# Performance work log

Hardware: AMD Instinct MI355X
Metric: run time of the kernel (lower is better)

The kernel has to match this reference:

```python
import jax, jax.numpy as jnp
import numpy as np

INFLUENCE_RADIUS = 8  # VectorizedTrajectoryComputer default


def compute_trajectories(emb):
    # emb: [B, S, D] -> [B, S, D]
    B, S, D = emb.shape
    diffs = emb[:, 1:] - emb[:, :-1]                      # [B, S-1, D]
    mag = jnp.linalg.norm(diffs, axis=-1, keepdims=True)  # [B, S-1, 1]
    ntraj = diffs / jnp.maximum(mag, 1e-8)                # normalized trajectories
    mw = jnp.tanh(mag[..., 0])                            # magnitude weights [B, S-1]
    pos = jnp.arange(S)[:, None]                          # [S, 1]
    j = jnp.arange(S - 1)[None, :]                        # [1, S-1]
    ws = jnp.maximum(0, pos - INFLUENCE_RADIUS)           # window start per pos
    mask = (j >= ws) & (j < pos)                          # window_end = pos (pos <= S-1)
    wsz = jnp.maximum(pos - ws, 1)                        # window size (>=1 to avoid /0)
    recency = jnp.where(mask, (j - ws + 1) / wsz, 0.0).astype(emb.dtype)  # [S, S-1]
    cw = mw[:, None, :] * recency[None]                   # combined weights [B, S, S-1]
    nw = cw / jnp.maximum(cw.sum(-1, keepdims=True), 1e-8)
    return jnp.einsum('bpj,bjd->bpd', nw, ntraj)          # [B, S, D]


def setup_inputs() -> dict:
    key = jax.random.key(0)
    ks = jax.random.split(key, 6)
    B, S, D = 2, 2048, 1024
    H, K, hd = 16, 16, 64
    return {
        'x': jax.random.normal(ks[0], (B, S, D), dtype=jnp.float32),
        'qkv_w': jax.random.normal(ks[1], (3 * D, D), dtype=jnp.float32) * 0.02,
        'out_w': jax.random.normal(ks[2], (D, D), dtype=jnp.float32) * 0.02,
        'splat_centers': jax.random.normal(ks[3], (H, K, hd), dtype=jnp.float32) * 0.02,
        'splat_log_scales': jnp.zeros((H, K), dtype=jnp.float32),
        'splat_amplitudes': jnp.ones((H, K), dtype=jnp.float32),
    }


def reference(x, qkv_w, out_w, splat_centers, splat_log_scales, splat_amplitudes):
    B, S, D = x.shape
    H, K, hd = splat_centers.shape
    # trajectories (computed when trajectories=None in forward)
    traj = compute_trajectories(x)
    # qkv projection (no bias)
    qkv = x @ qkv_w.T                                      # [B, S, 3D]
    q, k, v = jnp.split(qkv, 3, axis=-1)
    def heads(t):
        return t.reshape(B, S, H, hd).transpose(0, 2, 1, 3)  # [B, H, S, hd]
    q, k, v = heads(q), heads(k), heads(v)
    # squared distances to splat centers: [B, H, S, K]
    cn = jnp.sum(splat_centers ** 2, axis=-1)              # [H, K]
    def dists_sq(t):
        tn = jnp.sum(t ** 2, axis=-1, keepdims=True)       # [B, H, S, 1]
        cross = jnp.einsum('bhsd,hkd->bhsk', t, splat_centers)
        return tn - 2.0 * cross + cn[None, :, None, :]
    scales_sq = jnp.exp(splat_log_scales)[None, :, None, :] ** 2  # [1, H, 1, K]
    amp = jax.nn.sigmoid(splat_amplitudes)[None, :, None, :]
    q_weights = jnp.exp(-0.5 * dists_sq(q) / scales_sq) * amp     # [B, H, S, K]
    k_weights = jnp.exp(-0.5 * dists_sq(k) / scales_sq) * amp
    attn = jnp.einsum('bhis,bhjs->bhij', q_weights, k_weights)    # [B, H, S, S]
    attn = jax.nn.softmax(attn, axis=-1)
    out = jnp.einsum('bhij,bhjd->bhid', attn, v)                  # [B, H, S, hd]
    out = out.transpose(0, 2, 1, 3).reshape(B, S, D) @ out_w.T    # [B, S, D]
    return out, traj
```

## Files before the change

kernel.cpp:

```cpp
#include <hip/hip_runtime.h>
#include <math.h>

#define SEQ 2048
#define DIM 1024
#define NB  2
#define NH  16

typedef __attribute__((ext_vector_type(8))) short short8;
typedef __attribute__((ext_vector_type(4))) float floatx4;
typedef __attribute__((ext_vector_type(16))) float floatx16;

__device__ __forceinline__ ushort f2bf(float f) {
    unsigned u = __float_as_uint(f);
    return (ushort)((u + 0x7FFFu + ((u >> 16) & 1u)) >> 16);
}
__device__ __forceinline__ float bf2f(ushort h) {
    return __uint_as_float(((unsigned)h) << 16);
}
__device__ __forceinline__ void gload16(const void* g, char* lds_base) {
    __builtin_amdgcn_global_load_lds(
        (const __attribute__((address_space(1))) void*)g,
        (__attribute__((address_space(3))) void*)lds_base, 16, 0, 0);
}
__device__ __forceinline__ unsigned cvtpk(float a, float b) {
    unsigned r;
    asm("v_cvt_pk_bf16_f32 %0, %1, %2" : "=v"(r) : "v"(a), "v"(b));
    return r;
}
__device__ __forceinline__ void plswap(unsigned &a, unsigned &b) {
    asm("v_permlane32_swap_b32 %0, %1" : "+v"(a), "+v"(b));
}

__global__ __launch_bounds__(256) void front_kernel(
    const float* __restrict__ x, const float* __restrict__ qkv_w,
    const float* __restrict__ out_w,
    ushort* __restrict__ xh, ushort* __restrict__ xl,
    ushort* __restrict__ wh, ushort* __restrict__ wlv,
    ushort* __restrict__ owh, ushort* __restrict__ owl,
    float* __restrict__ sbuf, float* __restrict__ invbuf)
{
    const int blk = blockIdx.x;
    if (blk < 4096) {
        int i = blk * 1024 + threadIdx.x * 4;
        float4 v = *(const float4*)(x + i);
        ushort4 h, l;
        h.x = f2bf(v.x); l.x = f2bf(v.x - bf2f(h.x));
        h.y = f2bf(v.y); l.y = f2bf(v.y - bf2f(h.y));
        h.z = f2bf(v.z); l.z = f2bf(v.z - bf2f(h.z));
        h.w = f2bf(v.w); l.w = f2bf(v.w - bf2f(h.w));
        *(ushort4*)(xh + i) = h;
        *(ushort4*)(xl + i) = l;
    } else if (blk < 6144) {
        int i = (blk - 4096) * 1024 + threadIdx.x * 4;
        float4 v = *(const float4*)(qkv_w + i);
        ushort4 o;
        o.x = f2bf(v.x); o.y = f2bf(v.y); o.z = f2bf(v.z); o.w = f2bf(v.w);
        *(ushort4*)(wh + i) = o;
    } else if (blk < 7168) {
        int i = (blk - 6144) * 1024 + threadIdx.x * 4;
        float4 v = *(const float4*)(qkv_w + 2097152 + i);
        ushort4 h, l;
        h.x = f2bf(v.x); l.x = f2bf(v.x - bf2f(h.x));
        h.y = f2bf(v.y); l.y = f2bf(v.y - bf2f(h.y));
        h.z = f2bf(v.z); l.z = f2bf(v.z - bf2f(h.z));
        h.w = f2bf(v.w); l.w = f2bf(v.w - bf2f(h.w));
        *(ushort4*)(wh + 2097152 + i) = h;
        *(ushort4*)(wlv + i) = l;
    } else if (blk < 8192) {
        const int wave = threadIdx.x >> 6;
        const int lane = threadIdx.x & 63;
        const int row  = (blk - 7168) * 4 + wave;
        const int NR = NB * (SEQ - 1);
        if (row >= NR) return;
        const int b = row / (SEQ - 1);
        const int j = row - b * (SEQ - 1);
        const float* x0 = x + ((size_t)(b * SEQ + j)) * DIM;
        const float* x1 = x0 + DIM;
        float sum = 0.f;
        #pragma unroll
        for (int q = 0; q < 4; ++q) {
            int idx = q * 256 + lane * 4;
            float4 a = *(const float4*)(x0 + idx);
            float4 c = *(const float4*)(x1 + idx);
            float dx = c.x-a.x, dy = c.y-a.y, dz = c.z-a.z, dw = c.w-a.w;
            sum += dx*dx + dy*dy + dz*dz + dw*dw;
        }
        #pragma unroll
        for (int off = 32; off > 0; off >>= 1) sum += __shfl_down(sum, off);
        if (lane == 0) {
            float mag = sqrtf(sum);
            sbuf[row]   = tanhf(mag);
            invbuf[row] = 1.0f / fmaxf(mag, 1e-8f);
        }
    } else {
        int i = (blk - 8192) * 1024 + threadIdx.x * 4;
        float4 v = *(const float4*)(out_w + i);
        ushort4 h, l;
        h.x = f2bf(v.x); l.x = f2bf(v.x - bf2f(h.x));
        h.y = f2bf(v.y); l.y = f2bf(v.y - bf2f(h.y));
        h.z = f2bf(v.z); l.z = f2bf(v.z - bf2f(h.z));
        h.w = f2bf(v.w); l.w = f2bf(v.w - bf2f(h.w));
        *(ushort4*)(owh + i) = h;
        *(ushort4*)(owl + i) = l;
    }
}

__device__ __forceinline__ void traj_body(
    int bp, const float* __restrict__ x, const float* __restrict__ sbuf,
    const float* __restrict__ invbuf, float* __restrict__ traj_out)
{
    const int b  = bp >> 11;
    const int p  = bp & (SEQ - 1);
    int ws = p - 8; if (ws < 0) ws = 0;
    const int wlen = p - ws;
    const float wsz = (float)((p - ws) > 1 ? (p - ws) : 1);
    const int base = b * (SEQ - 1) + ws;

    float Z = 0.f;
    for (int t = 0; t < wlen; ++t)
        Z += sbuf[base + t] * ((float)(t + 1) / wsz);
    const float scale = 1.0f / fmaxf(Z, 1e-8f);

    const int d0 = threadIdx.x * 4;
    const float* xb = x + ((size_t)(b * SEQ + ws)) * DIM + d0;
    float4 prev = *(const float4*)xb;
    float4 acc = make_float4(0.f,0.f,0.f,0.f);
    for (int t = 0; t < wlen; ++t) {
        xb += DIM;
        float4 cur = *(const float4*)xb;
        float cc = sbuf[base + t] * ((float)(t + 1) / wsz) * invbuf[base + t] * scale;
        acc.x += cc * (cur.x - prev.x);
        acc.y += cc * (cur.y - prev.y);
        acc.z += cc * (cur.z - prev.z);
        acc.w += cc * (cur.w - prev.w);
        prev = cur;
    }
    *(float4*)(traj_out + (size_t)bp * DIM + d0) = acc;
}

template<int SPLIT, int EPI, int BN>
__device__ __forceinline__ void gemm_body(
    int bx, int by, char* smem,
    const ushort* __restrict__ Ah, const ushort* __restrict__ Al,
    const ushort* __restrict__ Bh, const ushort* __restrict__ Bl,
    float* __restrict__ cout, int ldc,
    ushort* __restrict__ qwb)
{
    constexpr int JT   = BN / 32;
    constexpr int BSZ  = BN * 64;
    constexpr int HALF = 8192 + BSZ;
    const int tid = threadIdx.x;
    const int l = tid & 63;
    const int w = tid >> 6;
    const int wm = w >> 1, wn = w & 1;
    const int n0 = bx * BN;
    const int m0 = by * 128;

    char* a_h = smem;
    char* b_h = smem + 8192;
    char* a_l = smem + HALF;
    char* b_l = smem + HALF + 8192;

    const int srowA = 32 * w + (l >> 2);
    const int srowB = (BN == 128 ? 32 * w : 16 * w) + (l >> 2);
    const int scol  = (l & 3) * 8;
    const ushort* Ahg = Ah + (size_t)(m0 + srowA) * 1024 + scol;
    const ushort* Bhg = Bh + (size_t)(n0 + srowB) * 1024 + scol;
    const ushort* Alg = SPLIT ? Al + (size_t)(m0 + srowA) * 1024 + scol : nullptr;
    const ushort* Blg = SPLIT ? Bl + (size_t)(n0 + srowB) * 1024 + scol : nullptr;

    floatx4 acc[4][JT] = {};
    const int fr = l & 15;
    const int fq = (l >> 4) * 16;

    for (int kb = 0; kb < 1024; kb += 32) {
        if (kb) __syncthreads();
        gload16(Ahg + kb,             a_h + w*2048);
        gload16(Ahg + kb + 16*1024,   a_h + w*2048 + 1024);
        if (BN == 128) {
            gload16(Bhg + kb,             b_h + w*2048);
            gload16(Bhg + kb + 16*1024,   b_h + w*2048 + 1024);
        } else {
            gload16(Bhg + kb,             b_h + w*1024);
        }
        if (SPLIT) {
            gload16(Alg + kb,           a_l + w*2048);
            gload16(Alg + kb + 16*1024, a_l + w*2048 + 1024);
            if (BN == 128) {
                gload16(Blg + kb,           b_l + w*2048);
                gload16(Blg + kb + 16*1024, b_l + w*2048 + 1024);
            } else {
                gload16(Blg + kb,           b_l + w*1024);
            }
        }
        __syncthreads();
        short8 fah[4], fbh[JT], fal[4], fbl[JT];
        #pragma unroll
        for (int t = 0; t < 4; ++t) {
            fah[t] = *(const short8*)(a_h + ((wm*64 + t*16 + fr) << 6) + fq);
            if (SPLIT)
                fal[t] = *(const short8*)(a_l + ((wm*64 + t*16 + fr) << 6) + fq);
        }
        #pragma unroll
        for (int t = 0; t < JT; ++t) {
            fbh[t] = *(const short8*)(b_h + ((wn*(BN/2) + t*16 + fr) << 6) + fq);
            if (SPLIT)
                fbl[t] = *(const short8*)(b_l + ((wn*(BN/2) + t*16 + fr) << 6) + fq);
        }
        #pragma unroll
        for (int it = 0; it < 4; ++it)
            #pragma unroll
            for (int jt = 0; jt < JT; ++jt) {
                acc[it][jt] = __builtin_amdgcn_mfma_f32_16x16x32_bf16(
                    fah[it], fbh[jt], acc[it][jt], 0, 0, 0);
                if (SPLIT) {
                    acc[it][jt] = __builtin_amdgcn_mfma_f32_16x16x32_bf16(
                        fah[it], fbl[jt], acc[it][jt], 0, 0, 0);
                    acc[it][jt] = __builtin_amdgcn_mfma_f32_16x16x32_bf16(
                        fal[it], fbh[jt], acc[it][jt], 0, 0, 0);
                }
            }
    }

    const int row0 = (l >> 4) * 4;
    const int col  = l & 15;

    if (EPI == 0) {
        #pragma unroll
        for (int it = 0; it < 4; ++it)
            #pragma unroll
            for (int jt = 0; jt < JT; ++jt)
                #pragma unroll
                for (int r = 0; r < 4; ++r) {
                    int gm = m0 + wm*64 + it*16 + row0 + r;
                    int gn = n0 + wn*(BN/2) + jt*16 + col;
                    cout[(size_t)gm * ldc + gn] = acc[it][jt][r];
                }
    } else {
        #pragma unroll
        for (int it = 0; it < 4; ++it)
            #pragma unroll
            for (int jt = 0; jt < JT; ++jt)
                #pragma unroll
                for (int r = 0; r < 4; ++r) {
                    int md = m0 + wm*64 + it*16 + row0 + r;
                    int t  = n0 + wn*(BN/2) + jt*16 + col;
                    int bb = t >> 11, ss = t & (SEQ - 1);
                    qwb[((size_t)bb << 21) + (size_t)md * SEQ + ss] = f2bf(acc[it][jt][r]);
                }
    }
}

__device__ __forceinline__ void qk_splat_body(
    int bx, int by, char* smem,
    const ushort* __restrict__ Ah, const ushort* __restrict__ Bh,
    ushort* __restrict__ qwb, ushort* __restrict__ kwb,
    const float* __restrict__ centers, const float* __restrict__ lscales,
    const float* __restrict__ amps)
{
    const int tid = threadIdx.x;
    const int l = tid & 63;
    const int w = tid >> 6;
    const int wm = w >> 1, wn = w & 1;
    const int n0 = bx * 128;
    const int m0 = by * 128;
    char* a_h = smem;
    char* b_h = smem + 8192;
    float* Cst = (float*)(smem + 32768);

    {
        const float* src = centers + (size_t)((n0 & 1023) >> 6) * 1024;
        float4 v0 = *(const float4*)(src + tid*8);
        float4 v1 = *(const float4*)(src + tid*8 + 4);
        *(float4*)(Cst + tid*8)     = v0;
        *(float4*)(Cst + tid*8 + 4) = v1;
    }

    const int srow = 32 * w + (l >> 2);
    const int scol = (l & 3) * 8;
    const ushort* Ahg = Ah + (size_t)(m0 + srow) * 1024 + scol;
    const ushort* Bhg = Bh + (size_t)(n0 + srow) * 1024 + scol;

    floatx4 acc[4][4] = {};
    const int fr = l & 15;
    const int fq = (l >> 4) * 16;

    for (int kb = 0; kb < 1024; kb += 32) {
        if (kb) __syncthreads();
        gload16(Ahg + kb,             a_h + w*2048);
        gload16(Ahg + kb + 16*1024,   a_h + w*2048 + 1024);
        gload16(Bhg + kb,             b_h + w*2048);
        gload16(Bhg + kb + 16*1024,   b_h + w*2048 + 1024);
        __syncthreads();
        short8 fah[4], fbh[4];
        #pragma unroll
        for (int t = 0; t < 4; ++t) {
            fah[t] = *(const short8*)(a_h + ((wm*64 + t*16 + fr) << 6) + fq);
            fbh[t] = *(const short8*)(b_h + ((wn*64 + t*16 + fr) << 6) + fq);
        }
        #pragma unroll
        for (int it = 0; it < 4; ++it)
            #pragma unroll
            for (int jt = 0; jt < 4; ++jt)
                acc[it][jt] = __builtin_amdgcn_mfma_f32_16x16x32_bf16(
                    fah[it], fbh[jt], acc[it][jt], 0, 0, 0);
    }

    __syncthreads();
    const int row0 = (l >> 4) * 4;
    const int col  = l & 15;
    ushort* qt = (ushort*)(smem + w*8192);

    #pragma unroll
    for (int it = 0; it < 4; ++it)
        #pragma unroll
        for (int jt = 0; jt < 4; ++jt)
            #pragma unroll
            for (int r = 0; r < 4; ++r) {
                int tok = it*16 + row0 + r;
                int c   = jt*16 + col;
                qt[tok*64 + ((((c >> 3) ^ (tok & 7)) << 3) | (c & 7))] =
                    f2bf(acc[it][jt][r]);
            }

    float qv[64];
    #pragma unroll
    for (int j = 0; j < 8; ++j) {
        short8 v = *(const short8*)(qt + l*64 + ((j ^ (l & 7)) << 3));
        #pragma unroll
        for (int i = 0; i < 8; ++i) qv[j*8 + i] = bf2f((ushort)v[i]);
    }

    const int hh = ((n0 & 1023) + wn*64) >> 6;
    const float* cw = Cst + wn*1024;
    const int tg = m0 + wm*64 + l;
    const int bb = tg >> 11, ss = tg & (SEQ - 1);
    ushort* obuf = (n0 < 1024) ? qwb : kwb;

    ushort o16[16];
    #pragma unroll
    for (int sp = 0; sp < 16; ++sp) {
        const float* cp = cw + sp*64;
        float dq = 0.f;
        #pragma unroll
        for (int i = 0; i < 64; ++i) {
            float t = qv[i] - cp[i];
            dq = fmaf(t, t, dq);
        }
        float s2 = __expf(2.f * lscales[hh*16 + sp]);
        float pa = 1.f / (1.f + __expf(-amps[hh*16 + sp]));
        o16[sp] = f2bf(__expf(dq * (-0.5f / s2)) * pa);
    }
    ushort* op = obuf + (((size_t)(bb*NH + hh))*SEQ + ss)*16;
    *(short8*)(op)     = *(short8*)(o16);
    *(short8*)(op + 8) = *(short8*)(o16 + 8);
}

__global__ __launch_bounds__(256) void mid_kernel(
    const ushort* __restrict__ xh, const ushort* __restrict__ xl,
    const ushort* __restrict__ wh, const ushort* __restrict__ wlv,
    ushort* __restrict__ vbt, ushort* __restrict__ qwb, ushort* __restrict__ kwb,
    const float* __restrict__ centers, const float* __restrict__ lscales,
    const float* __restrict__ amps,
    const float* __restrict__ x, const float* __restrict__ sbuf,
    const float* __restrict__ invb, float* __restrict__ traj_out)
{
    __shared__ __align__(16) char smem[40960];
    const int blk = blockIdx.x;
    if (blk < 512) {
        gemm_body<1,2,64>(blk & 63, blk >> 6, smem,
                          wh + 2048*1024, wlv, xh, xl, nullptr, 0, vbt);
    } else if (blk < 1024) {
        const int g = blk - 512;
        qk_splat_body(g & 15, g >> 4, smem, xh, wh,
                      qwb, kwb, centers, lscales, amps);
    } else {
        traj_body(blk - 1024, x, sbuf, invb, traj_out);
    }
}

__global__ __launch_bounds__(256) void gemmO_kernel(
    const ushort* __restrict__ Ah, const ushort* __restrict__ Al,
    const ushort* __restrict__ Bh, const ushort* __restrict__ Bl,
    float* __restrict__ cout)
{
    __shared__ __align__(16) char smem[2 * (8192 + 64*64)];
    gemm_body<1,0,64>(blockIdx.x, blockIdx.y, smem, Ah, Al, Bh, Bl,
                      cout, 1024, nullptr);
}

__global__ __launch_bounds__(256, 4) void attn_kernel(
    const ushort* __restrict__ qw, const ushort* __restrict__ kw,
    const ushort* __restrict__ vbt, ushort* __restrict__ hoh, ushort* __restrict__ hol)
{
    __shared__ __align__(16) char smem[16384 + 512];
    const int tid = threadIdx.x;
    const int l   = tid & 63;
    const int w   = tid >> 6;
    const int qh  = w >> 1;
    const int kh  = w & 1;
    const int l31 = l & 31;
    const int hi  = l >> 5;
    const int bh = blockIdx.y;
    const int b = bh >> 4;
    const int h = bh & 15;
    const int s0 = blockIdx.x * 64;

    short8 qf = *(const short8*)(qw + ((size_t)bh*SEQ + s0 + qh*32 + l31)*16 + hi*8);

    const ushort* kfp = kw + ((size_t)bh*SEQ + kh*32 + l31)*16 + hi*8;
    const ushort* vtb = vbt + ((size_t)(b*1024 + h*64))*SEQ;

    const int dA = w*16 + (l >> 3);
    const int dB = dA + 8;
    const ushort* vsA = vtb + (size_t)dA*SEQ + ((l & 7) ^ (dA & 7))*8;
    const ushort* vsB = vtb + (size_t)dB*SEQ + ((l & 7) ^ (dB & 7))*8;

    floatx16 acc0 = {}, acc1 = {};
    floatx16 zero16 = {};
    float zpart = 0.f;

    gload16(vsA, smem + w*2048);
    gload16(vsB, smem + w*2048 + 1024);
    short8 kf = *(const short8*)kfp;

    for (int jt = 0; jt < 32; ++jt) {
        __syncthreads();
        char* bufn = smem + ((jt + 1) & 1)*8192;
        if (jt < 31) {
            gload16(vsA + (jt + 1)*64, bufn + w*2048);
            gload16(vsB + (jt + 1)*64, bufn + w*2048 + 1024);
        }
        floatx16 sc = __builtin_amdgcn_mfma_f32_32x32x16_bf16(kf, qf, zero16, 0, 0, 0);
        if (jt < 31) kf = *(const short8*)(kfp + (jt + 1)*1024);

        float e[16];
        #pragma unroll
        for (int r = 0; r < 16; ++r) e[r] = __expf(sc[r]);
        float zs = 0.f;
        #pragma unroll
        for (int r = 0; r < 16; ++r) zs += e[r];
        zpart += zs;

        unsigned p0 = cvtpk(e[0],  e[1]),  p1 = cvtpk(e[2],  e[3]);
        unsigned p2 = cvtpk(e[4],  e[5]),  p3 = cvtpk(e[6],  e[7]);
        unsigned p4 = cvtpk(e[8],  e[9]),  p5 = cvtpk(e[10], e[11]);
        unsigned p6 = cvtpk(e[12], e[13]), p7 = cvtpk(e[14], e[15]);
        plswap(p0, p2); plswap(p1, p3);
        plswap(p4, p6); plswap(p5, p7);
        union { unsigned u[4]; short8 s; } ua, ub;
        ua.u[0] = p0; ua.u[1] = p1; ua.u[2] = p2; ua.u[3] = p3;
        ub.u[0] = p4; ub.u[1] = p5; ub.u[2] = p6; ub.u[3] = p7;

        const ushort* buf = (const ushort*)(smem + (jt & 1)*8192);
        #pragma unroll
        for (int dt = 0; dt < 2; ++dt) {
            int row = dt*32 + l31;
            const ushort* vr = buf + row*64;
            int bk0 = (kh*4 + hi)     ^ (row & 7);
            int bk1 = (kh*4 + 2 + hi) ^ (row & 7);
            short8 vb0 = *(const short8*)(vr + bk0*8);
            short8 vb1 = *(const short8*)(vr + bk1*8);
            if (dt == 0) {
                acc0 = __builtin_amdgcn_mfma_f32_32x32x16_bf16(ua.s, vb0, acc0, 0, 0, 0);
                acc0 = __builtin_amdgcn_mfma_f32_32x32x16_bf16(ub.s, vb1, acc0, 0, 0, 0);
            } else {
                acc1 = __builtin_amdgcn_mfma_f32_32x32x16_bf16(ua.s, vb0, acc1, 0, 0, 0);
                acc1 = __builtin_amdgcn_mfma_f32_32x32x16_bf16(ub.s, vb1, acc1, 0, 0, 0);
            }
        }
    }

    __syncthreads();

    float* cb = (float*)smem;
    float* zb = (float*)(smem + 16384);

    unsigned za = __float_as_uint(zpart), zc = za;
    plswap(za, zc);
    float zq = __uint_as_float(za) + __uint_as_float(zc);
    if (l31 == l) zb[kh*64 + qh*32 + l31] = zq;

    if (kh) {
        #pragma unroll
        for (int r = 0; r < 16; ++r) {
            int q = (r & 3) + 8*(r >> 2) + 4*hi;
            cb[(qh*32 + q)*64 + l31]      = acc0[r];
            cb[(qh*32 + q)*64 + 32 + l31] = acc1[r];
        }
    }
    __syncthreads();
    if (!kh) {
        #pragma unroll
        for (int r = 0; r < 16; ++r) {
            int q = (r & 3) + 8*(r >> 2) + 4*hi;
            float zt = zb[qh*32 + q] + zb[64 + qh*32 + q];
            float inv = 1.0f / zt;
            int s = s0 + qh*32 + q;
            size_t base = ((size_t)(b*SEQ + s))*1024 + h*64;
            float v0 = (acc0[r] + cb[(qh*32 + q)*64 + l31])      * inv;
            float v1 = (acc1[r] + cb[(qh*32 + q)*64 + 32 + l31]) * inv;
            ushort h0 = f2bf(v0);
            ushort h1 = f2bf(v1);
            hoh[base + l31]      = h0;
            hol[base + l31]      = f2bf(v0 - bf2f(h0));
            hoh[base + 32 + l31] = h1;
            hol[base + 32 + l31] = f2bf(v1 - bf2f(h1));
        }
    }
}

extern "C" void kernel_launch(void* const* d_in, const int* in_sizes, int n_in,
                              void* d_out, int out_size, void* d_ws, size_t ws_size,
                              hipStream_t stream)
{
    const float* x       = (const float*)d_in[0];
    const float* qkv_w   = (const float*)d_in[1];
    const float* out_w   = (const float*)d_in[2];
    const float* centers = (const float*)d_in[3];
    const float* lscales = (const float*)d_in[4];
    const float* amps    = (const float*)d_in[5];
    float* out  = (float*)d_out;
    float* traj = out + (size_t)NB*SEQ*DIM;

    char* wsb = (char*)d_ws;
    ushort* xh   = (ushort*)(wsb);
    ushort* xl   = (ushort*)(wsb + (8u<<20));
    ushort* wh   = (ushort*)(wsb + (16u<<20));
    ushort* wlv  = (ushort*)(wsb + (22u<<20));
    ushort* vbt  = (ushort*)(wsb + (24u<<20));
    ushort* owh  = (ushort*)(wsb + (32u<<20));
    ushort* owl  = (ushort*)(wsb + (34u<<20));
    ushort* qwbh = (ushort*)(wsb + (36u<<20));
    ushort* kwbh = (ushort*)(wsb + (38u<<20));
    float*  sbuf = (float*)(wsb + (40u<<20));
    float*  invb = sbuf + 4096;
    ushort* hoh  = xh;
    ushort* hol  = xl;

    front_kernel<<<9216, 256, 0, stream>>>(
        x, qkv_w, out_w, xh, xl, wh, wlv, owh, owl, sbuf, invb);
    mid_kernel<<<5120, 256, 0, stream>>>(
        xh, xl, wh, wlv, vbt, qwbh, kwbh, centers, lscales, amps,
        x, sbuf, invb, traj);
    attn_kernel<<<dim3(32, 32), 256, 0, stream>>>(qwbh, kwbh, vbt, hoh, hol);
    gemmO_kernel<<<dim3(16, 32), 256, 0, stream>>>(hoh, hol, owh, owl, out);
}
```

Before: 255.9 us.

## Split mid kernel by LDS need and restructure splat distance loop

The fused mid kernel is split into two launches. The V GEMM shares its launch with most trajectory blocks and uses a smaller LDS footprint, while the QK-splat blocks get their own launch with the remaining trajectory blocks. This means the light blocks are no longer limited to the occupancy set by the 40 KB allocation. The splat distance computation now streams 8-element chunks of q against all 16 centers, so the 64-float qv register array is gone. Per-splat scale and amplitude constants are precomputed once into shared memory instead of computing exp and sigmoid per thread. The cost is an extra kernel launch and a dependency boundary between the two halves.

```diff
diff --git a/kernel.cpp b/kernel.cpp
--- a/kernel.cpp
+++ b/kernel.cpp
@@ -267,13 +267,21 @@
     char* a_h = smem;
     char* b_h = smem + 8192;
     float* Cst = (float*)(smem + 32768);
-
+    float* Pr  = (float*)(smem + 40960);
+
+    const int hb = (n0 & 1023) >> 6;
     {
-        const float* src = centers + (size_t)((n0 & 1023) >> 6) * 1024;
+        const float* src = centers + (size_t)hb * 1024;
         float4 v0 = *(const float4*)(src + tid*8);
         float4 v1 = *(const float4*)(src + tid*8 + 4);
         *(float4*)(Cst + tid*8)     = v0;
         *(float4*)(Cst + tid*8 + 4) = v1;
+    }
+    if (tid < 32) {
+        int hl = tid >> 4, sp = tid & 15;
+        float s2 = __expf(2.f * lscales[(hb + hl)*16 + sp]);
+        Pr[hl*32 + sp]      = -0.5f / s2;
+        Pr[hl*32 + 16 + sp] = 1.f / (1.f + __expf(-amps[(hb + hl)*16 + sp]));
     }
 
     const int srow = 32 * w + (l >> 2);
@@ -323,59 +331,79 @@
                     f2bf(acc[it][jt][r]);
             }
 
-    float qv[64];
+    const float* cw  = Cst + wn*1024;
+    const float* prc = Pr  + wn*32;
+    float dq[16];
     #pragma unroll
-    for (int j = 0; j < 8; ++j) {
-        short8 v = *(const short8*)(qt + l*64 + ((j ^ (l & 7)) << 3));
-        #pragma unroll
-        for (int i = 0; i < 8; ++i) qv[j*8 + i] = bf2f((ushort)v[i]);
-    }
-
-    const int hh = ((n0 & 1023) + wn*64) >> 6;
-    const float* cw = Cst + wn*1024;
+    for (int sp = 0; sp < 16; ++sp) dq[sp] = 0.f;
+
+    #pragma unroll
+    for (int cb = 0; cb < 8; ++cb) {
+        short8 v = *(const short8*)(qt + l*64 + ((cb ^ (l & 7)) << 3));
+        float qv8[8];
+        #pragma unroll
+        for (int i = 0; i < 8; ++i) qv8[i] = bf2f((ushort)v[i]);
+        const float* cbp = cw + cb*8;
+        #pragma unroll
+        for (int sp = 0; sp < 16; ++sp) {
+            float4 c0 = *(const float4*)(cbp + sp*64);
+            float4 c1 = *(const float4*)(cbp + sp*64 + 4);
+            float t0 = qv8[0] - c0.x; dq[sp] = fmaf(t0, t0, dq[sp]);
+            float t1 = qv8[1] - c0.y; dq[sp] = fmaf(t1, t1, dq[sp]);
+            float t2 = qv8[2] - c0.z; dq[sp] = fmaf(t2, t2, dq[sp]);
+            float t3 = qv8[3] - c0.w; dq[sp] = fmaf(t3, t3, dq[sp]);
+            float t4 = qv8[4] - c1.x; dq[sp] = fmaf(t4, t4, dq[sp]);
+            float t5 = qv8[5] - c1.y; dq[sp] = fmaf(t5, t5, dq[sp]);
+            float t6 = qv8[6] - c1.z; dq[sp] = fmaf(t6, t6, dq[sp]);
+            float t7 = qv8[7] - c1.w; dq[sp] = fmaf(t7, t7, dq[sp]);
+        }
+    }
+
+    const int hh = hb + wn;
     const int tg = m0 + wm*64 + l;
     const int bb = tg >> 11, ss = tg & (SEQ - 1);
     ushort* obuf = (n0 < 1024) ? qwb : kwb;
-
     ushort o16[16];
     #pragma unroll
-    for (int sp = 0; sp < 16; ++sp) {
-        const float* cp = cw + sp*64;
-        float dq = 0.f;
-        #pragma unroll
-        for (int i = 0; i < 64; ++i) {
-            float t = qv[i] - cp[i];
-            dq = fmaf(t, t, dq);
-        }
-        float s2 = __expf(2.f * lscales[hh*16 + sp]);
-        float pa = 1.f / (1.f + __expf(-amps[hh*16 + sp]));
-        o16[sp] = f2bf(__expf(dq * (-0.5f / s2)) * pa);
-    }
+    for (int sp = 0; sp < 16; ++sp)
+        o16[sp] = f2bf(__expf(dq[sp] * prc[sp]) * prc[16 + sp]);
     ushort* op = obuf + (((size_t)(bb*NH + hh))*SEQ + ss)*16;
     *(short8*)(op)     = *(short8*)(o16);
     *(short8*)(op + 8) = *(short8*)(o16 + 8);
 }
 
-__global__ __launch_bounds__(256) void mid_kernel(
-    const ushort* __restrict__ xh, const ushort* __restrict__ xl,
-    const ushort* __restrict__ wh, const ushort* __restrict__ wlv,
-    ushort* __restrict__ vbt, ushort* __restrict__ qwb, ushort* __restrict__ kwb,
+__global__ __launch_bounds__(256) void gemmV_traj_kernel(
+    const ushort* __restrict__ Ah, const ushort* __restrict__ Al,
+    const ushort* __restrict__ Bh, const ushort* __restrict__ Bl,
+    ushort* __restrict__ vbt,
+    const float* __restrict__ x, const float* __restrict__ sbuf,
+    const float* __restrict__ invbuf, float* __restrict__ traj_out)
+{
+    __shared__ __align__(16) char smem[2 * (8192 + 64*64)];
+    const int blk = blockIdx.x;
+    if (blk < 512) {
+        gemm_body<1,2,64>(blk & 63, blk >> 6, smem, Ah, Al, Bh, Bl,
+                          nullptr, 0, vbt);
+    } else {
+        traj_body(blk - 512, x, sbuf, invbuf, traj_out);
+    }
+}
+
+__global__ __launch_bounds__(256) void qksplat_traj_kernel(
+    const ushort* __restrict__ Ah, const ushort* __restrict__ Bh,
+    ushort* __restrict__ qwb, ushort* __restrict__ kwb,
     const float* __restrict__ centers, const float* __restrict__ lscales,
     const float* __restrict__ amps,
     const float* __restrict__ x, const float* __restrict__ sbuf,
-    const float* __restrict__ invb, float* __restrict__ traj_out)
-{
-    __shared__ __align__(16) char smem[40960];
+    const float* __restrict__ invbuf, float* __restrict__ traj_out)
+{
+    __shared__ __align__(16) char smem[41216];
     const int blk = blockIdx.x;
     if (blk < 512) {
-        gemm_body<1,2,64>(blk & 63, blk >> 6, smem,
-                          wh + 2048*1024, wlv, xh, xl, nullptr, 0, vbt);
-    } else if (blk < 1024) {
-        const int g = blk - 512;
-        qk_splat_body(g & 15, g >> 4, smem, xh, wh,
+        qk_splat_body(blk & 15, blk >> 4, smem, Ah, Bh,
                       qwb, kwb, centers, lscales, amps);
     } else {
-        traj_body(blk - 1024, x, sbuf, invb, traj_out);
+        traj_body(blk - 512 + 3072, x, sbuf, invbuf, traj_out);
     }
 }
 
@@ -540,9 +568,10 @@
 
     front_kernel<<<9216, 256, 0, stream>>>(
         x, qkv_w, out_w, xh, xl, wh, wlv, owh, owl, sbuf, invb);
-    mid_kernel<<<5120, 256, 0, stream>>>(
-        xh, xl, wh, wlv, vbt, qwbh, kwbh, centers, lscales, amps,
-        x, sbuf, invb, traj);
+    gemmV_traj_kernel<<<3584, 256, 0, stream>>>(
+        wh + 2048*1024, wlv, xh, xl, vbt, x, sbuf, invb, traj);
+    qksplat_traj_kernel<<<1536, 256, 0, stream>>>(
+        xh, wh, qwbh, kwbh, centers, lscales, amps, x, sbuf, invb, traj);
     attn_kernel<<<dim3(32, 32), 256, 0, stream>>>(qwbh, kwbh, vbt, hoh, hol);
     gemmO_kernel<<<dim3(16, 32), 256, 0, stream>>>(hoh, hol, owh, owl, out);
 }
```

Measured after the change: 233.3 us, median of 2. 8.8% less time.
